# Kernel tuning notes

Measured on AMD Instinct MI355X. Metric: run time of the kernel, lower is better.

## Reference

```python
import jax, jax.numpy as jnp
import numpy as np

B, H, S, D = 2, 16, 2048, 64


def setup_inputs() -> dict:
    key = jax.random.key(0)
    kq, kk, kv = jax.random.split(key, 3)
    query = jax.random.normal(kq, (B, H, S, D), dtype=jnp.float32)
    k = jax.random.normal(kk, (B, H, S, D), dtype=jnp.float32)
    value = jax.random.normal(kv, (B, H, S, D), dtype=jnp.float32)
    # causal boolean mask, broadcast over heads: (B, 1, S, S)
    mask = jnp.broadcast_to(jnp.tril(jnp.ones((S, S), dtype=bool)), (B, 1, S, S))
    return {"query": query, "key": k, "value": value, "mask": mask}


def reference(query, key, value, mask):
    # scores: (B, H, Sq, Sk)
    dim = query.shape[-1]
    scale = 1.0 / jnp.sqrt(jnp.asarray(dim, dtype=query.dtype))
    scores = jnp.einsum('bhqd,bhkd->bhqk', query, key) * scale
    scores = jnp.where(mask, scores, jnp.asarray(-jnp.inf, dtype=scores.dtype))
    attn = jax.nn.softmax(scores, axis=-1)
    # dropout is identity in eval mode (reference is deterministic)
    out = jnp.einsum('bhqk,bhkd->bhqd', attn, value)
    return out
```

## Files before the change

### kernel.cpp

```cpp
#include <hip/hip_runtime.h>
#include <hip/hip_bf16.h>
#include <math.h>


#define S_LEN 2048
#define D_DIM 64
#define QSCALE 0.18033688f

typedef float f32x16 __attribute__((ext_vector_type(16)));
typedef __bf16 bf16x8 __attribute__((ext_vector_type(8)));
typedef unsigned int uint2v __attribute__((ext_vector_type(2)));

static __device__ inline unsigned int cvtpk(float lo, float hi) {
  unsigned int r;
  asm("v_cvt_pk_bf16_f32 %0, %1, %2" : "=v"(r) : "v"(lo), "v"(hi));
  return r;
}
static __device__ inline float fexp2(float x) {
#if __has_builtin(__builtin_amdgcn_exp2f)
  return __builtin_amdgcn_exp2f(x);
#else
  float r;
  asm("v_exp_f32 %0, %1\n\ts_nop 1" : "=v"(r) : "v"(x));
  return r;
#endif
}
static __device__ inline void gload_lds16(const void* g, void* l) {
  __builtin_amdgcn_global_load_lds(
      (const __attribute__((address_space(1))) void*)g,
      (__attribute__((address_space(3))) void*)l, 16, 0, 0);
}

__global__ __launch_bounds__(256) void attn_prep_kernel(
    const float* __restrict__ K, const float* __restrict__ V,
    unsigned short* __restrict__ ws) {
  __shared__ float kl[64][65];
  __shared__ float vt[64][65];
  const int bt = (int)blockIdx.x;
  const int bh = bt >> 5, tile = bt & 31;
  const float* Kt = K + ((size_t)bh * S_LEN + tile * 64) * D_DIM;
  const float* Vt = V + ((size_t)bh * S_LEN + tile * 64) * D_DIM;
  unsigned short* wk = ws + (size_t)bt * 8192;
  unsigned short* wv = wk + 4096;
  const int t = threadIdx.x;
  const int r = t >> 2, cg = (t & 3) * 16;
#pragma unroll
  for (int i = 0; i < 4; ++i) {
    float4 f = *(const float4*)(Kt + r * 64 + cg + i * 4);
    kl[r][cg + i * 4 + 0] = f.x; kl[r][cg + i * 4 + 1] = f.y;
    kl[r][cg + i * 4 + 2] = f.z; kl[r][cg + i * 4 + 3] = f.w;
    float4 g = *(const float4*)(Vt + r * 64 + cg + i * 4);
    vt[cg + i * 4 + 0][r] = g.x; vt[cg + i * 4 + 1][r] = g.y;
    vt[cg + i * 4 + 2][r] = g.z; vt[cg + i * 4 + 3][r] = g.w;
  }
  __syncthreads();
  const int lane = t & 63, wv4 = t >> 6;
  const int fr = lane & 31, fc = (lane >> 5) * 8;
#pragma unroll
  for (int fp = 0; fp < 2; ++fp) {
    const int fid = fp * 4 + wv4;
    const int kc = fid >> 1, mt = fid & 1;
    bf16x8 kb, vb;
#pragma unroll
    for (int j = 0; j < 8; ++j) {
      kb[j] = (__bf16)kl[mt * 32 + fr][kc * 16 + fc + j];
      vb[j] = (__bf16)vt[(fid & 1) * 32 + fr][(fid >> 1) * 16 + fc + j];
    }
    *(bf16x8*)(wk + ((size_t)fid * 64 + lane) * 8) = kb;
    *(bf16x8*)(wv + ((size_t)fid * 64 + lane) * 8) = vb;
  }
}

__global__ __launch_bounds__(256, 2) void attn_fwd_frag(
    const float* __restrict__ Qg, const unsigned short* __restrict__ ws,
    float* __restrict__ Og) {
  __shared__ unsigned short lds_kv[2][16384];

  const int t = threadIdx.x;
  const int lane = t & 63, qt = t >> 6, l31 = lane & 31, h = lane >> 5;

  const int wgid = (int)blockIdx.x;
  const int xcd = wgid & 7, idx = wgid >> 3;
  const int slot = (idx & 31) >> 2;
  const int grp = (idx < 32) ? (15 - slot) : slot;
  const int bh = xcd * 4 + (idx & 3);
  const size_t base = (size_t)bh * S_LEN * D_DIM;
  const float* Q = Qg + base;
  float*       O = Og + base;
  const unsigned short* wsh = ws + (size_t)bh * 32 * 8192;
  const int loff = lane * 8;

  const int strip = grp * 4 + qt;
  const int q0 = strip * 32;
  const int qg = q0 + l31;
  const int mynit = (strip >> 1) + 1;
  const int npair = grp + 1;

  bf16x8 qf[4];
  {
    const float* qp = Q + (size_t)qg * D_DIM + h * 8;
#pragma unroll
    for (int kc = 0; kc < 4; ++kc) {
      float4 a = *(const float4*)(qp + kc * 16);
      float4 b = *(const float4*)(qp + kc * 16 + 4);
      bf16x8 q8;
      q8[0] = (__bf16)(a.x * QSCALE); q8[1] = (__bf16)(a.y * QSCALE);
      q8[2] = (__bf16)(a.z * QSCALE); q8[3] = (__bf16)(a.w * QSCALE);
      q8[4] = (__bf16)(b.x * QSCALE); q8[5] = (__bf16)(b.y * QSCALE);
      q8[6] = (__bf16)(b.z * QSCALE); q8[7] = (__bf16)(b.w * QSCALE);
      qf[kc] = q8;
    }
  }
  const uint4 ou = { 0x3F803F80u, 0x3F803F80u, 0x3F803F80u, 0x3F803F80u };
  const bf16x8 ones = __builtin_bit_cast(bf16x8, ou);

  f32x16 acc0 = (f32x16)0.0f, acc1 = (f32x16)0.0f;
  f32x16 sacc = (f32x16)0.0f;

  auto stage = [&](int buf, int pair) {
    const unsigned short* src = wsh + (size_t)pair * 16384 + qt * 512 + loff;
    unsigned short* dst = &lds_kv[buf][qt * 512 + loff];
#pragma unroll
    for (int r = 0; r < 8; ++r)
      gload_lds16(src + r * 2048, dst + r * 2048);
  };

  stage(0, 0);
  __syncthreads();

  for (int it = 0; it < npair; ++it) {
    const int cur = it & 1;
    if (it + 1 < npair) stage(cur ^ 1, it + 1);

#pragma unroll
    for (int sub = 0; sub < 2; ++sub) {
      const int tt = it * 2 + sub;
      if (tt >= mynit) break;
      const unsigned short* lk = &lds_kv[cur][sub * 8192];
      const unsigned short* lv = lk + 4096;

      f32x16 st[2];
      st[0] = (f32x16)0.0f; st[1] = (f32x16)0.0f;
#pragma unroll
      for (int kc = 0; kc < 4; ++kc) {
#pragma unroll
        for (int mt = 0; mt < 2; ++mt) {
          bf16x8 kf = *(const bf16x8*)(lk + (kc * 2 + mt) * 512 + loff);
          st[mt] = __builtin_amdgcn_mfma_f32_32x32x16_bf16(kf, qf[kc], st[mt], 0, 0, 0);
        }
      }

      if (tt == mynit - 1) {
        const int kv0 = tt * 64;
#pragma unroll
        for (int mt = 0; mt < 2; ++mt)
#pragma unroll
          for (int r = 0; r < 16; ++r) {
            int kv = kv0 + mt * 32 + (r & 3) + 8 * (r >> 2) + 4 * h;
            st[mt][r] = (kv <= qg) ? st[mt][r] : -INFINITY;
          }
      }

#pragma unroll
      for (int mt = 0; mt < 2; ++mt)
#pragma unroll
        for (int r = 0; r < 16; ++r)
          st[mt][r] = fexp2(st[mt][r]);

#pragma unroll
      for (int cc = 0; cc < 4; ++cc) {
        const int rb = 8 * (cc & 1);
        const int m2 = cc >> 1;
        unsigned int A0 = cvtpk(st[m2][rb + 0], st[m2][rb + 1]);
        unsigned int A1 = cvtpk(st[m2][rb + 2], st[m2][rb + 3]);
        unsigned int B0 = cvtpk(st[m2][rb + 4], st[m2][rb + 5]);
        unsigned int B1 = cvtpk(st[m2][rb + 6], st[m2][rb + 7]);
        unsigned int W0, W1, W2, W3;
#if __has_builtin(__builtin_amdgcn_permlane32_swap)
        {
          uint2v r02 = __builtin_amdgcn_permlane32_swap(A0, B0, false, false);
          uint2v r13 = __builtin_amdgcn_permlane32_swap(A1, B1, false, false);
          W0 = r02[0]; W2 = r02[1];
          W1 = r13[0]; W3 = r13[1];
        }
#else
        {
          unsigned int sA0 = (unsigned int)__shfl_xor((int)A0, 32);
          unsigned int sB0 = (unsigned int)__shfl_xor((int)B0, 32);
          unsigned int sA1 = (unsigned int)__shfl_xor((int)A1, 32);
          unsigned int sB1 = (unsigned int)__shfl_xor((int)B1, 32);
          W0 = h ? sB0 : A0;  W2 = h ? B0 : sA0;
          W1 = h ? sB1 : A1;  W3 = h ? B1 : sA1;
        }
#endif
        uint4 uw = { W0, W1, W2, W3 };
        bf16x8 pa = __builtin_bit_cast(bf16x8, uw);
        bf16x8 v0 = *(const bf16x8*)(lv + (cc * 2 + 0) * 512 + loff);
        bf16x8 v1 = *(const bf16x8*)(lv + (cc * 2 + 1) * 512 + loff);
        acc0 = __builtin_amdgcn_mfma_f32_32x32x16_bf16(pa, v0,   acc0, 0, 0, 0);
        acc1 = __builtin_amdgcn_mfma_f32_32x32x16_bf16(pa, v1,   acc1, 0, 0, 0);
        sacc = __builtin_amdgcn_mfma_f32_32x32x16_bf16(pa, ones, sacc, 0, 0, 0);
      }
    }
    __syncthreads();
  }

#pragma unroll
  for (int r = 0; r < 16; ++r) {
    const int mrow = (r & 3) + 8 * (r >> 2) + 4 * h;
    const float inv = 1.0f / sacc[r];
    float* op = O + (size_t)(q0 + mrow) * D_DIM + l31;
    op[0]  = acc0[r] * inv;
    op[32] = acc1[r] * inv;
  }
}

extern "C" void kernel_launch(void* const* d_in, const int* in_sizes, int n_in,
                              void* d_out, int out_size, void* d_ws, size_t ws_size,
                              hipStream_t stream) {
  const float* q = (const float*)d_in[0];
  const float* k = (const float*)d_in[1];
  const float* v = (const float*)d_in[2];
  float* o = (float*)d_out;
  unsigned short* ws = (unsigned short*)d_ws;
  attn_prep_kernel<<<1024, 256, 0, stream>>>(k, v, ws);
  attn_fwd_frag<<<512, 256, 0, stream>>>(q, ws, o);
}
```

Before: 43.98 us.

## Split KV range across wave pairs and pair strips per block for balance

Each block now handles two 64-row query chunks (c and 31-c) in two phases, which balances causal work across blocks. Within a phase, two waves share each 32-row strip and take alternating (even/odd) KV tiles. Their partial accumulators and row sums are then merged through swizzled LDS before normalisation and the store. This removes per-wave idle time from uneven causal iteration counts, at the cost of an LDS reduction, extra barriers and reloading Q per phase.

```diff
diff --git a/kernel.cpp b/kernel.cpp
--- a/kernel.cpp
+++ b/kernel.cpp
@@ -8,6 +8,7 @@
 #define QSCALE 0.18033688f
 
 typedef float f32x16 __attribute__((ext_vector_type(16)));
+typedef float f32x4v __attribute__((ext_vector_type(4)));
 typedef __bf16 bf16x8 __attribute__((ext_vector_type(8)));
 typedef unsigned int uint2v __attribute__((ext_vector_type(2)));
 
@@ -78,44 +79,22 @@
 
   const int t = threadIdx.x;
   const int lane = t & 63, qt = t >> 6, l31 = lane & 31, h = lane >> 5;
+  const int sl = qt >> 1;
+  const int par = qt & 1;
+  const int lsw = lane & 7;
 
   const int wgid = (int)blockIdx.x;
   const int xcd = wgid & 7, idx = wgid >> 3;
-  const int slot = (idx & 31) >> 2;
-  const int grp = (idx < 32) ? (15 - slot) : slot;
   const int bh = xcd * 4 + (idx & 3);
+  const int c = idx >> 2;
   const size_t base = (size_t)bh * S_LEN * D_DIM;
   const float* Q = Qg + base;
   float*       O = Og + base;
   const unsigned short* wsh = ws + (size_t)bh * 32 * 8192;
   const int loff = lane * 8;
 
-  const int strip = grp * 4 + qt;
-  const int q0 = strip * 32;
-  const int qg = q0 + l31;
-  const int mynit = (strip >> 1) + 1;
-  const int npair = grp + 1;
-
-  bf16x8 qf[4];
-  {
-    const float* qp = Q + (size_t)qg * D_DIM + h * 8;
-#pragma unroll
-    for (int kc = 0; kc < 4; ++kc) {
-      float4 a = *(const float4*)(qp + kc * 16);
-      float4 b = *(const float4*)(qp + kc * 16 + 4);
-      bf16x8 q8;
-      q8[0] = (__bf16)(a.x * QSCALE); q8[1] = (__bf16)(a.y * QSCALE);
-      q8[2] = (__bf16)(a.z * QSCALE); q8[3] = (__bf16)(a.w * QSCALE);
-      q8[4] = (__bf16)(b.x * QSCALE); q8[5] = (__bf16)(b.y * QSCALE);
-      q8[6] = (__bf16)(b.z * QSCALE); q8[7] = (__bf16)(b.w * QSCALE);
-      qf[kc] = q8;
-    }
-  }
   const uint4 ou = { 0x3F803F80u, 0x3F803F80u, 0x3F803F80u, 0x3F803F80u };
   const bf16x8 ones = __builtin_bit_cast(bf16x8, ou);
-
-  f32x16 acc0 = (f32x16)0.0f, acc1 = (f32x16)0.0f;
-  f32x16 sacc = (f32x16)0.0f;
 
   auto stage = [&](int buf, int pair) {
     const unsigned short* src = wsh + (size_t)pair * 16384 + qt * 512 + loff;
@@ -125,93 +104,148 @@
       gload_lds16(src + r * 2048, dst + r * 2048);
   };
 
-  stage(0, 0);
-  __syncthreads();
-
-  for (int it = 0; it < npair; ++it) {
-    const int cur = it & 1;
-    if (it + 1 < npair) stage(cur ^ 1, it + 1);
-
-#pragma unroll
-    for (int sub = 0; sub < 2; ++sub) {
-      const int tt = it * 2 + sub;
-      if (tt >= mynit) break;
-      const unsigned short* lk = &lds_kv[cur][sub * 8192];
-      const unsigned short* lv = lk + 4096;
-
-      f32x16 st[2];
-      st[0] = (f32x16)0.0f; st[1] = (f32x16)0.0f;
+  for (int ph = 0; ph < 2; ++ph) {
+    const int jj = ph ? c : (31 - c);
+    const int strip = 2 * jj + sl;
+    const int q0 = strip * 32;
+    const int qg = q0 + l31;
+    const int nint = (jj >> 1) + 1;
+
+    bf16x8 qf[4];
+    {
+      const float* qp = Q + (size_t)qg * D_DIM + h * 8;
 #pragma unroll
       for (int kc = 0; kc < 4; ++kc) {
-#pragma unroll
-        for (int mt = 0; mt < 2; ++mt) {
-          bf16x8 kf = *(const bf16x8*)(lk + (kc * 2 + mt) * 512 + loff);
-          st[mt] = __builtin_amdgcn_mfma_f32_32x32x16_bf16(kf, qf[kc], st[mt], 0, 0, 0);
-        }
-      }
-
-      if (tt == mynit - 1) {
-        const int kv0 = tt * 64;
+        float4 a = *(const float4*)(qp + kc * 16);
+        float4 b = *(const float4*)(qp + kc * 16 + 4);
+        bf16x8 q8;
+        q8[0] = (__bf16)(a.x * QSCALE); q8[1] = (__bf16)(a.y * QSCALE);
+        q8[2] = (__bf16)(a.z * QSCALE); q8[3] = (__bf16)(a.w * QSCALE);
+        q8[4] = (__bf16)(b.x * QSCALE); q8[5] = (__bf16)(b.y * QSCALE);
+        q8[6] = (__bf16)(b.z * QSCALE); q8[7] = (__bf16)(b.w * QSCALE);
+        qf[kc] = q8;
+      }
+    }
+
+    f32x16 acc0 = (f32x16)0.0f, acc1 = (f32x16)0.0f;
+    f32x16 sacc = (f32x16)0.0f;
+
+    stage(0, 0);
+    __syncthreads();
+
+    for (int i = 0; i < nint; ++i) {
+      const int cur = i & 1;
+      if (i + 1 < nint) stage(cur ^ 1, i + 1);
+
+      const int tt = 2 * i + par;
+      if (tt <= jj) {
+        const unsigned short* lk = &lds_kv[cur][par * 8192];
+        const unsigned short* lv = lk + 4096;
+
+        f32x16 st[2];
+        st[0] = (f32x16)0.0f; st[1] = (f32x16)0.0f;
+#pragma unroll
+        for (int kc = 0; kc < 4; ++kc) {
+#pragma unroll
+          for (int mt = 0; mt < 2; ++mt) {
+            bf16x8 kf = *(const bf16x8*)(lk + (kc * 2 + mt) * 512 + loff);
+            st[mt] = __builtin_amdgcn_mfma_f32_32x32x16_bf16(kf, qf[kc], st[mt], 0, 0, 0);
+          }
+        }
+
+        if (tt == jj) {
+          const int kv0 = tt * 64;
+#pragma unroll
+          for (int mt = 0; mt < 2; ++mt)
+#pragma unroll
+            for (int r = 0; r < 16; ++r) {
+              int kv = kv0 + mt * 32 + (r & 3) + 8 * (r >> 2) + 4 * h;
+              st[mt][r] = (kv <= qg) ? st[mt][r] : -INFINITY;
+            }
+        }
+
 #pragma unroll
         for (int mt = 0; mt < 2; ++mt)
 #pragma unroll
-          for (int r = 0; r < 16; ++r) {
-            int kv = kv0 + mt * 32 + (r & 3) + 8 * (r >> 2) + 4 * h;
-            st[mt][r] = (kv <= qg) ? st[mt][r] : -INFINITY;
+          for (int r = 0; r < 16; ++r)
+            st[mt][r] = fexp2(st[mt][r]);
+
+#pragma unroll
+        for (int cc = 0; cc < 4; ++cc) {
+          const int rb = 8 * (cc & 1);
+          const int m2 = cc >> 1;
+          unsigned int A0 = cvtpk(st[m2][rb + 0], st[m2][rb + 1]);
+          unsigned int A1 = cvtpk(st[m2][rb + 2], st[m2][rb + 3]);
+          unsigned int B0 = cvtpk(st[m2][rb + 4], st[m2][rb + 5]);
+          unsigned int B1 = cvtpk(st[m2][rb + 6], st[m2][rb + 7]);
+          unsigned int W0, W1, W2, W3;
+#if __has_builtin(__builtin_amdgcn_permlane32_swap)
+          {
+            uint2v r02 = __builtin_amdgcn_permlane32_swap(A0, B0, false, false);
+            uint2v r13 = __builtin_amdgcn_permlane32_swap(A1, B1, false, false);
+            W0 = r02[0]; W2 = r02[1];
+            W1 = r13[0]; W3 = r13[1];
           }
-      }
-
-#pragma unroll
-      for (int mt = 0; mt < 2; ++mt)
-#pragma unroll
-        for (int r = 0; r < 16; ++r)
-          st[mt][r] = fexp2(st[mt][r]);
-
-#pragma unroll
-      for (int cc = 0; cc < 4; ++cc) {
-        const int rb = 8 * (cc & 1);
-        const int m2 = cc >> 1;
-        unsigned int A0 = cvtpk(st[m2][rb + 0], st[m2][rb + 1]);
-        unsigned int A1 = cvtpk(st[m2][rb + 2], st[m2][rb + 3]);
-        unsigned int B0 = cvtpk(st[m2][rb + 4], st[m2][rb + 5]);
-        unsigned int B1 = cvtpk(st[m2][rb + 6], st[m2][rb + 7]);
-        unsigned int W0, W1, W2, W3;
-#if __has_builtin(__builtin_amdgcn_permlane32_swap)
-        {
-          uint2v r02 = __builtin_amdgcn_permlane32_swap(A0, B0, false, false);
-          uint2v r13 = __builtin_amdgcn_permlane32_swap(A1, B1, false, false);
-          W0 = r02[0]; W2 = r02[1];
-          W1 = r13[0]; W3 = r13[1];
-        }
 #else
-        {
-          unsigned int sA0 = (unsigned int)__shfl_xor((int)A0, 32);
-          unsigned int sB0 = (unsigned int)__shfl_xor((int)B0, 32);
-          unsigned int sA1 = (unsigned int)__shfl_xor((int)A1, 32);
-          unsigned int sB1 = (unsigned int)__shfl_xor((int)B1, 32);
-          W0 = h ? sB0 : A0;  W2 = h ? B0 : sA0;
-          W1 = h ? sB1 : A1;  W3 = h ? B1 : sA1;
-        }
+          {
+            unsigned int sA0 = (unsigned int)__shfl_xor((int)A0, 32);
+            unsigned int sB0 = (unsigned int)__shfl_xor((int)B0, 32);
+            unsigned int sA1 = (unsigned int)__shfl_xor((int)A1, 32);
+            unsigned int sB1 = (unsigned int)__shfl_xor((int)B1, 32);
+            W0 = h ? sB0 : A0;  W2 = h ? B0 : sA0;
+            W1 = h ? sB1 : A1;  W3 = h ? B1 : sA1;
+          }
 #endif
-        uint4 uw = { W0, W1, W2, W3 };
-        bf16x8 pa = __builtin_bit_cast(bf16x8, uw);
-        bf16x8 v0 = *(const bf16x8*)(lv + (cc * 2 + 0) * 512 + loff);
-        bf16x8 v1 = *(const bf16x8*)(lv + (cc * 2 + 1) * 512 + loff);
-        acc0 = __builtin_amdgcn_mfma_f32_32x32x16_bf16(pa, v0,   acc0, 0, 0, 0);
-        acc1 = __builtin_amdgcn_mfma_f32_32x32x16_bf16(pa, v1,   acc1, 0, 0, 0);
-        sacc = __builtin_amdgcn_mfma_f32_32x32x16_bf16(pa, ones, sacc, 0, 0, 0);
+          uint4 uw = { W0, W1, W2, W3 };
+          bf16x8 pa = __builtin_bit_cast(bf16x8, uw);
+          bf16x8 v0 = *(const bf16x8*)(lv + (cc * 2 + 0) * 512 + loff);
+          bf16x8 v1 = *(const bf16x8*)(lv + (cc * 2 + 1) * 512 + loff);
+          acc0 = __builtin_amdgcn_mfma_f32_32x32x16_bf16(pa, v0,   acc0, 0, 0, 0);
+          acc1 = __builtin_amdgcn_mfma_f32_32x32x16_bf16(pa, v1,   acc1, 0, 0, 0);
+          sacc = __builtin_amdgcn_mfma_f32_32x32x16_bf16(pa, ones, sacc, 0, 0, 0);
+        }
+      }
+      __syncthreads();
+    }
+
+    float* mb = reinterpret_cast<float*>(&lds_kv[0][0]);
+    if (par == 1) {
+      float* a = mb + (sl * 64 + lane) * 48;
+#pragma unroll
+      for (int rg = 0; rg < 4; ++rg) {
+        f32x4v v0 = { acc0[rg * 4 + 0], acc0[rg * 4 + 1], acc0[rg * 4 + 2], acc0[rg * 4 + 3] };
+        f32x4v v1 = { acc1[rg * 4 + 0], acc1[rg * 4 + 1], acc1[rg * 4 + 2], acc1[rg * 4 + 3] };
+        f32x4v vs = { sacc[rg * 4 + 0], sacc[rg * 4 + 1], sacc[rg * 4 + 2], sacc[rg * 4 + 3] };
+        *(f32x4v*)&a[(rg ^ lsw) * 4]       = v0;
+        *(f32x4v*)&a[((rg + 4) ^ lsw) * 4] = v1;
+        *(f32x4v*)&a[32 + rg * 4]          = vs;
       }
     }
     __syncthreads();
-  }
-
-#pragma unroll
-  for (int r = 0; r < 16; ++r) {
-    const int mrow = (r & 3) + 8 * (r >> 2) + 4 * h;
-    const float inv = 1.0f / sacc[r];
-    float* op = O + (size_t)(q0 + mrow) * D_DIM + l31;
-    op[0]  = acc0[r] * inv;
-    op[32] = acc1[r] * inv;
+    if (par == 0) {
+      const float* a = mb + (sl * 64 + lane) * 48;
+#pragma unroll
+      for (int rg = 0; rg < 4; ++rg) {
+        f32x4v v0 = *(const f32x4v*)&a[(rg ^ lsw) * 4];
+        f32x4v v1 = *(const f32x4v*)&a[((rg + 4) ^ lsw) * 4];
+        f32x4v vs = *(const f32x4v*)&a[32 + rg * 4];
+#pragma unroll
+        for (int j = 0; j < 4; ++j) {
+          acc0[rg * 4 + j] += v0[j];
+          acc1[rg * 4 + j] += v1[j];
+          sacc[rg * 4 + j] += vs[j];
+        }
+      }
+#pragma unroll
+      for (int r = 0; r < 16; ++r) {
+        const int mrow = (r & 3) + 8 * (r >> 2) + 4 * h;
+        const float inv = 1.0f / sacc[r];
+        float* op = O + (size_t)(q0 + mrow) * D_DIM + l31;
+        op[0]  = acc0[r] * inv;
+        op[32] = acc1[r] * inv;
+      }
+    }
+    __syncthreads();
   }
 }
 
```

Result: no change. 43.81 us (-0.4%).
